# Performance work log

Measured on AMD Instinct MI355X. Metric: run time of the kernel, lower is better.

## Reference

```python
import jax, jax.numpy as jnp
import numpy as np

DIM = 1024
KV_DIM = 1024
WINDOW_SIZE = 64  # band half-width = 32, band width W = 65
B, S = 2, 2048


def setup_inputs() -> dict:
    key = jax.random.key(0)
    ks = jax.random.split(key, 12)
    w_scale = 1.0 / np.sqrt(DIM)
    return {
        "x": jax.random.normal(ks[0], (B, S, DIM), dtype=jnp.float32),
        # neural_memory: Linear(dim, kv) -> ReLU -> Linear(kv, dim); weights stored [in, out]
        "nm_w1": jax.random.normal(ks[1], (DIM, KV_DIM), dtype=jnp.float32) * w_scale,
        "nm_b1": jnp.zeros((KV_DIM,), dtype=jnp.float32),
        "nm_w2": jax.random.normal(ks[2], (KV_DIM, DIM), dtype=jnp.float32) * w_scale,
        "nm_b2": jnp.zeros((DIM,), dtype=jnp.float32),
        # SlidingWindowAttention projections (dim -> dim)
        "q_w": jax.random.normal(ks[3], (DIM, DIM), dtype=jnp.float32) * w_scale,
        "q_b": jnp.zeros((DIM,), dtype=jnp.float32),
        "k_w": jax.random.normal(ks[4], (DIM, DIM), dtype=jnp.float32) * w_scale,
        "k_b": jnp.zeros((DIM,), dtype=jnp.float32),
        "v_w": jax.random.normal(ks[5], (DIM, DIM), dtype=jnp.float32) * w_scale,
        "v_b": jnp.zeros((DIM,), dtype=jnp.float32),
    }


def _sliding_window_attention(m, q_w, q_b, k_w, k_b, v_w, v_b, window_size):
    # m: [B, S, D]. Per position i, attend to [i - w//2, i + w//2] inclusive.
    Bsz, Seq, D = m.shape
    q = m @ q_w + q_b
    k = m @ k_w + k_b
    v = m @ v_w + v_b
    half = window_size // 2
    offsets = jnp.arange(-half, half + 1)                # [W]
    idx = jnp.arange(Seq)[:, None] + offsets[None, :]    # [S, W]
    valid = (idx >= 0) & (idx < Seq)                     # [S, W]
    idx_c = jnp.clip(idx, 0, Seq - 1)
    k_band = k[:, idx_c]                                 # [B, S, W, D]
    v_band = v[:, idx_c]                                 # [B, S, W, D]
    scale = 1.0 / jnp.sqrt(jnp.float32(D))
    scores = jnp.einsum("bsd,bswd->bsw", q, k_band) * scale
    scores = jnp.where(valid[None, :, :], scores, -jnp.inf)
    weights = jax.nn.softmax(scores, axis=-1)            # [B, S, W]
    return jnp.einsum("bsw,bswd->bsd", weights, v_band)


def reference(x, nm_w1, nm_b1, nm_w2, nm_b2, q_w, q_b, k_w, k_b, v_w, v_b):
    # Faithful output path of LongTermMemory.forward: the key/value-proj MSE
    # surprise update mutates key_proj weights in-place (no_grad) but does NOT
    # affect the returned tensor o, which is swa(neural_memory(x)).
    h = jax.nn.relu(x @ nm_w1 + nm_b1)
    m = h @ nm_w2 + nm_b2                                # neural_memory(x): [B, S, D]
    return _sliding_window_attention(m, q_w, q_b, k_w, k_b, v_w, v_b, WINDOW_SIZE)
```

## Files before the change

kernel.cpp:

```cpp
#include <hip/hip_runtime.h>
#include <cstdint>

#define DIMN 1024
#define SEQ  2048
#define BATCH 2
#define MTOT (BATCH*SEQ)
#define NELEM_ACT (MTOT*DIMN)
#define NELEM_W   (DIMN*DIMN)

typedef __attribute__((ext_vector_type(8))) short   s16x8;
typedef __attribute__((ext_vector_type(4))) float   f32x4v;

__device__ __forceinline__ float b2f(unsigned short u) {
  union { unsigned int i; float f; } x; x.i = ((unsigned int)u) << 16; return x.f;
}
__device__ __forceinline__ unsigned short f2b(float f) {
  unsigned int x = __float_as_uint(f);
  return (unsigned short)((x + 0x7fffu + ((x >> 16) & 1u)) >> 16);
}

__device__ __forceinline__ void gload16(const void* g, void* l) {
  __builtin_amdgcn_global_load_lds((const __attribute__((address_space(1))) void*)g,
                                   (__attribute__((address_space(3))) void*)l,
                                   16, 0, 0);
}

__global__ __launch_bounds__(256) void cvt_kernel(
    const float* __restrict__ in, unsigned short* __restrict__ out, int n) {
  int i = (blockIdx.x * 256 + threadIdx.x) * 8;
  if (i >= n) return;
  float4 v0 = *(const float4*)(in + i);
  float4 v1 = *(const float4*)(in + i + 4);
  ushort4 a, b;
  a.x = f2b(v0.x); a.y = f2b(v0.y); a.z = f2b(v0.z); a.w = f2b(v0.w);
  b.x = f2b(v1.x); b.y = f2b(v1.y); b.z = f2b(v1.z); b.w = f2b(v1.w);
  *(ushort4*)(out + i) = a;
  *(ushort4*)(out + i + 4) = b;
}

__global__ __launch_bounds__(256) void transpose5_kernel(
    const float* __restrict__ w1, const float* __restrict__ w2,
    const float* __restrict__ qw, const float* __restrict__ kw,
    const float* __restrict__ vw,
    unsigned short* __restrict__ w1t, unsigned short* __restrict__ w2t,
    unsigned short* __restrict__ wqkvt) {
  __shared__ float t[32][33];
  int z = blockIdx.z;
  const float* in = (z == 0) ? w1 : (z == 1) ? w2 : (z == 2) ? qw : (z == 3) ? kw : vw;
  unsigned short* dst = (z == 0) ? w1t : (z == 1) ? w2t : wqkvt + (size_t)(z - 2) * NELEM_W;

  int tx = threadIdx.x & 31, ty = threadIdx.x >> 5;
  int r0 = blockIdx.y * 32, c0 = blockIdx.x * 32;
  #pragma unroll
  for (int i = 0; i < 32; i += 8)
    t[ty + i][tx] = in[(size_t)(r0 + ty + i) * DIMN + c0 + tx];
  __syncthreads();
  #pragma unroll
  for (int i = 0; i < 32; i += 8)
    dst[(size_t)(c0 + ty + i) * DIMN + r0 + tx] = f2b(t[tx][ty + i]);
}

template<int EPI>
__global__ __launch_bounds__(256) void gemm_kernel(
    const unsigned short* __restrict__ A, const unsigned short* __restrict__ Bt,
    const float* __restrict__ bias0, const float* __restrict__ bias1,
    const float* __restrict__ bias2,
    unsigned short* __restrict__ O, int Ndim, int Kdim) {
  __shared__ unsigned short lds[16 * 512];

  const int tid  = threadIdx.x;
  const int lane = tid & 63;
  const int wave = tid >> 6;
  const int wm = wave >> 1;
  const int wn = wave & 1;
  const int frow = lane & 15;
  const int krow = lane >> 4;
  const int bm0 = blockIdx.y * 128;
  const int bn0 = blockIdx.x * 128;

  f32x4v acc[4][4] = {};

  for (int k0 = 0; k0 < Kdim; k0 += 32) {
    for (int i = wave; i < 16; i += 4) {
      const unsigned short* src = (i < 8) ? A : Bt;
      int row = (i < 8) ? (bm0 + i * 16 + frow) : (bn0 + (i - 8) * 16 + frow);
      gload16(src + (size_t)row * Kdim + k0 + krow * 8, lds + i * 512);
    }
    __syncthreads();

    const short* sl = (const short*)lds;
    s16x8 a[4], b[4];
    #pragma unroll
    for (int m = 0; m < 4; ++m)
      a[m] = *(const s16x8*)(sl + (wm * 4 + m) * 512 + lane * 8);
    #pragma unroll
    for (int n = 0; n < 4; ++n)
      b[n] = *(const s16x8*)(sl + (8 + wn * 4 + n) * 512 + lane * 8);

    #pragma unroll
    for (int m = 0; m < 4; ++m)
      #pragma unroll
      for (int n = 0; n < 4; ++n)
        acc[m][n] = __builtin_amdgcn_mfma_f32_16x16x32_bf16(a[m], b[n], acc[m][n], 0, 0, 0);
    __syncthreads();
  }

  #pragma unroll
  for (int n = 0; n < 4; ++n) {
    int col = bn0 + wn * 64 + n * 16 + frow;
    float bv;
    if (EPI == 2) {
      int sel = col >> 10;
      const float* bp = (sel == 0) ? bias0 : (sel == 1) ? bias1 : bias2;
      bv = bp[col & (DIMN - 1)];
    } else {
      bv = bias0[col];
    }
    #pragma unroll
    for (int m = 0; m < 4; ++m) {
      int rbase = bm0 + wm * 64 + m * 16 + krow * 4;
      #pragma unroll
      for (int r = 0; r < 4; ++r) {
        float v = acc[m][n][r] + bv;
        if (EPI == 0) v = fmaxf(v, 0.f);
        O[(size_t)(rbase + r) * Ndim + col] = f2b(v);
      }
    }
  }
}

__global__ __launch_bounds__(256) void attn_kernel(
    const unsigned short* __restrict__ qkv, float* __restrict__ out) {
  __shared__ float sc[72];
  __shared__ float wts[72];
  __shared__ float part[4][16][68];
  const float NEG_INF = -__builtin_huge_valf();
  const int ROWS = 3 * DIMN;

  int bs = blockIdx.x;
  int s = bs & (SEQ - 1);
  int tid = threadIdx.x, lane = tid & 63, wave = tid >> 6;

  float qr[16];
  {
    const unsigned short* qp = qkv + (size_t)bs * ROWS + lane * 16;
    s16x8 q0 = *(const s16x8*)qp;
    s16x8 q1 = *(const s16x8*)(qp + 8);
    #pragma unroll
    for (int i = 0; i < 8; ++i) {
      qr[i]     = b2f((unsigned short)q0[i]) * 0.03125f;
      qr[8 + i] = b2f((unsigned short)q1[i]) * 0.03125f;
    }
  }

  const unsigned short* kbase = qkv + (size_t)(bs - s) * ROWS + DIMN;
  for (int j = wave; j < 65; j += 4) {
    int pos = s - 32 + j;
    float dot;
    if (pos >= 0 && pos < SEQ) {
      const unsigned short* kp = kbase + (size_t)pos * ROWS + lane * 16;
      s16x8 k0 = *(const s16x8*)kp;
      s16x8 k1 = *(const s16x8*)(kp + 8);
      dot = 0.f;
      #pragma unroll
      for (int i = 0; i < 8; ++i)
        dot += qr[i] * b2f((unsigned short)k0[i]) + qr[8 + i] * b2f((unsigned short)k1[i]);
      #pragma unroll
      for (int off = 32; off > 0; off >>= 1) dot += __shfl_xor(dot, off);
    } else {
      dot = NEG_INF;
    }
    if (lane == 0) sc[j] = dot;
  }
  __syncthreads();

  if (wave == 0) {
    float v0 = sc[lane];
    float v1 = (lane == 0) ? sc[64] : NEG_INF;
    float mx = fmaxf(v0, v1);
    #pragma unroll
    for (int off = 32; off > 0; off >>= 1) mx = fmaxf(mx, __shfl_xor(mx, off));
    float p0 = __expf(v0 - mx);
    float p1 = (lane == 0) ? __expf(v1 - mx) : 0.f;
    float sm = p0 + p1;
    #pragma unroll
    for (int off = 32; off > 0; off >>= 1) sm += __shfl_xor(sm, off);
    float inv = 1.f / sm;
    wts[lane] = p0 * inv;
    if (lane == 0) wts[64] = p1 * inv;
  }
  __syncthreads();

  float acc[16];
  #pragma unroll
  for (int i = 0; i < 16; ++i) acc[i] = 0.f;
  const unsigned short* vbase = qkv + (size_t)(bs - s) * ROWS + 2 * DIMN;
  for (int j = wave; j < 65; j += 4) {
    int pos = s - 32 + j;
    if (pos < 0 || pos >= SEQ) continue;
    float w = wts[j];
    const unsigned short* vp = vbase + (size_t)pos * ROWS + lane * 16;
    s16x8 v0 = *(const s16x8*)vp;
    s16x8 v1 = *(const s16x8*)(vp + 8);
    #pragma unroll
    for (int i = 0; i < 8; ++i) {
      acc[i]     += w * b2f((unsigned short)v0[i]);
      acc[8 + i] += w * b2f((unsigned short)v1[i]);
    }
  }
  #pragma unroll
  for (int i = 0; i < 16; ++i) part[wave][i][lane] = acc[i];
  __syncthreads();

  int d0 = tid * 4;
  int lsrc = d0 >> 4;
  int ibase = d0 & 15;
  float r0 = 0.f, r1 = 0.f, r2 = 0.f, r3 = 0.f;
  #pragma unroll
  for (int w = 0; w < 4; ++w) {
    r0 += part[w][ibase + 0][lsrc];
    r1 += part[w][ibase + 1][lsrc];
    r2 += part[w][ibase + 2][lsrc];
    r3 += part[w][ibase + 3][lsrc];
  }
  float4 r; r.x = r0; r.y = r1; r.z = r2; r.w = r3;
  *(float4*)(out + (size_t)bs * DIMN + d0) = r;
}

extern "C" void kernel_launch(void* const* d_in, const int* in_sizes, int n_in,
                              void* d_out, int out_size, void* d_ws, size_t ws_size,
                              hipStream_t stream) {
  const float* x  = (const float*)d_in[0];
  const float* w1 = (const float*)d_in[1];
  const float* b1 = (const float*)d_in[2];
  const float* w2 = (const float*)d_in[3];
  const float* b2 = (const float*)d_in[4];
  const float* qw = (const float*)d_in[5];
  const float* qb = (const float*)d_in[6];
  const float* kw = (const float*)d_in[7];
  const float* kb = (const float*)d_in[8];
  const float* vw = (const float*)d_in[9];
  const float* vb = (const float*)d_in[10];
  float* out = (float*)d_out;

  char* ws = (char*)d_ws;
  const size_t MB = 1024 * 1024;
  unsigned short* x_bf  = (unsigned short*)(ws);
  unsigned short* h_bf  = (unsigned short*)(ws + 8 * MB);
  unsigned short* qkv   = (unsigned short*)(ws);
  unsigned short* m_bf  = (unsigned short*)(ws + 24 * MB);
  unsigned short* w1t   = (unsigned short*)(ws + 32 * MB);
  unsigned short* w2t   = (unsigned short*)(ws + 34 * MB);
  unsigned short* wqkvt = (unsigned short*)(ws + 36 * MB);

  cvt_kernel<<<NELEM_ACT / (256 * 8), 256, 0, stream>>>(x, x_bf, NELEM_ACT);
  transpose5_kernel<<<dim3(32, 32, 5), 256, 0, stream>>>(w1, w2, qw, kw, vw,
                                                         w1t, w2t, wqkvt);

  dim3 g1(DIMN / 128, MTOT / 128);
  gemm_kernel<0><<<g1, 256, 0, stream>>>(x_bf, w1t, b1, nullptr, nullptr,
                                         h_bf, DIMN, DIMN);
  gemm_kernel<1><<<g1, 256, 0, stream>>>(h_bf, w2t, b2, nullptr, nullptr,
                                         m_bf, DIMN, DIMN);
  dim3 g2(3 * DIMN / 128, MTOT / 128);
  gemm_kernel<2><<<g2, 256, 0, stream>>>(m_bf, wqkvt, qb, kb, vb,
                                         qkv, 3 * DIMN, DIMN);

  attn_kernel<<<MTOT, 256, 0, stream>>>(qkv, out);
}
```

Baseline: 272.4 us.

## Rewrite sliding-window attention with MFMA blocks and retile GEMMs with K=64 steps

Replaces the per-token scalar attention kernel with a block kernel that handles 32 queries per workgroup. It computes the banded QK scores and the PV products with bf16 MFMA over a 96-key window, and the QKV GEMM epilogue writes V transposed so it can serve as the MFMA B operand. The GEMM kernel is templated on tile shape, uses a 64-deep K step per barrier pair, and the first two GEMMs move to 64x128 tiles for more workgroups. The band scheme computes about 50% redundant scores and quantizes the probabilities to bf16, and the transposed V stores are strided.

Result: faster. 242.1 us (-11.2%).

```diff
diff --git a/kernel.cpp b/kernel.cpp
--- a/kernel.cpp
+++ b/kernel.cpp
@@ -60,13 +60,15 @@
     dst[(size_t)(c0 + ty + i) * DIMN + r0 + tx] = f2b(t[tx][ty + i]);
 }
 
-template<int EPI>
+template<int MF, int NF, int EPI>
 __global__ __launch_bounds__(256) void gemm_kernel(
     const unsigned short* __restrict__ A, const unsigned short* __restrict__ Bt,
     const float* __restrict__ bias0, const float* __restrict__ bias1,
     const float* __restrict__ bias2,
-    unsigned short* __restrict__ O, int Ndim, int Kdim) {
-  __shared__ unsigned short lds[16 * 512];
+    unsigned short* __restrict__ O, unsigned short* __restrict__ O2,
+    int Ndim, int Kdim) {
+  constexpr int TB = (MF + NF) * 4;
+  __shared__ unsigned short lds[TB * 512];
 
   const int tid  = threadIdx.x;
   const int lane = tid & 63;
@@ -75,39 +77,50 @@
   const int wn = wave & 1;
   const int frow = lane & 15;
   const int krow = lane >> 4;
-  const int bm0 = blockIdx.y * 128;
-  const int bn0 = blockIdx.x * 128;
-
-  f32x4v acc[4][4] = {};
-
-  for (int k0 = 0; k0 < Kdim; k0 += 32) {
-    for (int i = wave; i < 16; i += 4) {
-      const unsigned short* src = (i < 8) ? A : Bt;
-      int row = (i < 8) ? (bm0 + i * 16 + frow) : (bn0 + (i - 8) * 16 + frow);
-      gload16(src + (size_t)row * Kdim + k0 + krow * 8, lds + i * 512);
+  const int bm0 = blockIdx.y * (MF * 32);
+  const int bn0 = blockIdx.x * (NF * 32);
+
+  f32x4v acc[MF][NF] = {};
+
+  for (int k0 = 0; k0 < Kdim; k0 += 64) {
+    #pragma unroll
+    for (int t = 0; t < TB / 4; ++t) {
+      int i = wave + t * 4;
+      const unsigned short* src;
+      if (i < MF * 4) {
+        int mf = i >> 1, ds = i & 1;
+        src = A + (size_t)(bm0 + mf * 16 + frow) * Kdim + k0 + ds * 32 + krow * 8;
+      } else {
+        int j = i - MF * 4;
+        int nf = j >> 1, ds = j & 1;
+        src = Bt + (size_t)(bn0 + nf * 16 + frow) * Kdim + k0 + ds * 32 + krow * 8;
+      }
+      gload16(src, lds + i * 512);
     }
     __syncthreads();
 
     const short* sl = (const short*)lds;
-    s16x8 a[4], b[4];
-    #pragma unroll
-    for (int m = 0; m < 4; ++m)
-      a[m] = *(const s16x8*)(sl + (wm * 4 + m) * 512 + lane * 8);
-    #pragma unroll
-    for (int n = 0; n < 4; ++n)
-      b[n] = *(const s16x8*)(sl + (8 + wn * 4 + n) * 512 + lane * 8);
-
-    #pragma unroll
-    for (int m = 0; m < 4; ++m)
-      #pragma unroll
-      for (int n = 0; n < 4; ++n)
-        acc[m][n] = __builtin_amdgcn_mfma_f32_16x16x32_bf16(a[m], b[n], acc[m][n], 0, 0, 0);
-    __syncthreads();
-  }
-
-  #pragma unroll
-  for (int n = 0; n < 4; ++n) {
-    int col = bn0 + wn * 64 + n * 16 + frow;
+    #pragma unroll
+    for (int ds = 0; ds < 2; ++ds) {
+      s16x8 a[MF], b[NF];
+      #pragma unroll
+      for (int m = 0; m < MF; ++m)
+        a[m] = *(const s16x8*)(sl + ((wm * MF + m) * 2 + ds) * 512 + lane * 8);
+      #pragma unroll
+      for (int n = 0; n < NF; ++n)
+        b[n] = *(const s16x8*)(sl + (MF * 4 + (wn * NF + n) * 2 + ds) * 512 + lane * 8);
+      #pragma unroll
+      for (int m = 0; m < MF; ++m)
+        #pragma unroll
+        for (int n = 0; n < NF; ++n)
+          acc[m][n] = __builtin_amdgcn_mfma_f32_16x16x32_bf16(a[m], b[n], acc[m][n], 0, 0, 0);
+    }
+    __syncthreads();
+  }
+
+  #pragma unroll
+  for (int n = 0; n < NF; ++n) {
+    int col = bn0 + wn * (NF * 16) + n * 16 + frow;
     float bv;
     if (EPI == 2) {
       int sel = col >> 10;
@@ -117,114 +130,173 @@
       bv = bias0[col];
     }
     #pragma unroll
-    for (int m = 0; m < 4; ++m) {
-      int rbase = bm0 + wm * 64 + m * 16 + krow * 4;
+    for (int m = 0; m < MF; ++m) {
+      int rbase = bm0 + wm * (MF * 16) + m * 16 + krow * 4;
+      if (EPI == 2 && col >= 2048) {
+        int d = col - 2048;
+        ushort4 pk;
+        pk.x = f2b(acc[m][n][0] + bv); pk.y = f2b(acc[m][n][1] + bv);
+        pk.z = f2b(acc[m][n][2] + bv); pk.w = f2b(acc[m][n][3] + bv);
+        *(ushort4*)(O2 + (size_t)d * MTOT + rbase) = pk;
+      } else {
+        #pragma unroll
+        for (int r = 0; r < 4; ++r) {
+          float v = acc[m][n][r] + bv;
+          if (EPI == 0) v = fmaxf(v, 0.f);
+          if (EPI == 2) O[(size_t)(rbase + r) * 2048 + col] = f2b(v);
+          else          O[(size_t)(rbase + r) * Ndim + col] = f2b(v);
+        }
+      }
+    }
+  }
+}
+
+#define QBLK 32
+#define NEGI (-1.0e30f)
+
+__global__ __launch_bounds__(256) void attn_mfma_kernel(
+    const unsigned short* __restrict__ qk,
+    const unsigned short* __restrict__ vt,
+    float* __restrict__ out) {
+  __shared__ unsigned short stage[24 * 512];
+  __shared__ unsigned short plds[QBLK][136];
+  __shared__ float pmax[2][QBLK];
+  __shared__ float psum[2][QBLK];
+
+  const int tid = threadIdx.x, lane = tid & 63, wave = tid >> 6;
+  const int frow = lane & 15, krow = lane >> 4;
+  const int tok0 = blockIdx.x * QBLK;
+  const int s0 = tok0 & (SEQ - 1);
+  const int bbase = tok0 - s0;
+  const int qf = wave & 1;
+  const int kh = wave >> 1;
+
+  f32x4v sacc[3] = {};
+  for (int d0 = 0; d0 < DIMN; d0 += 64) {
+    #pragma unroll
+    for (int t = 0; t < 4; ++t) {
+      int i = wave + t * 4;
+      const unsigned short* src;
+      if (i < 4) {
+        int qfs = i >> 1, ds = i & 1;
+        src = qk + (size_t)(tok0 + qfs * 16 + frow) * 2048 + d0 + ds * 32 + krow * 8;
+      } else {
+        int j = i - 4;
+        int kf = j >> 1, ds = j & 1;
+        int kpos = s0 - 32 + kf * 16 + frow;
+        kpos = min(max(kpos, 0), SEQ - 1);
+        src = qk + (size_t)(bbase + kpos) * 2048 + 1024 + d0 + ds * 32 + krow * 8;
+      }
+      gload16(src, stage + i * 512);
+    }
+    __syncthreads();
+    const short* sl = (const short*)stage;
+    #pragma unroll
+    for (int ds = 0; ds < 2; ++ds) {
+      s16x8 bq = *(const s16x8*)(sl + (qf * 2 + ds) * 512 + lane * 8);
+      #pragma unroll
+      for (int f = 0; f < 3; ++f) {
+        int kf = kh * 3 + f;
+        s16x8 ak = *(const s16x8*)(sl + (4 + kf * 2 + ds) * 512 + lane * 8);
+        sacc[f] = __builtin_amdgcn_mfma_f32_16x16x32_bf16(ak, bq, sacc[f], 0, 0, 0);
+      }
+    }
+    __syncthreads();
+  }
+
+  const int qloc = qf * 16 + frow;
+  const int qpos = s0 + qloc;
+  float sv[3][4];
+  float mx = NEGI;
+  #pragma unroll
+  for (int f = 0; f < 3; ++f) {
+    #pragma unroll
+    for (int r = 0; r < 4; ++r) {
+      int kloc = (kh * 3 + f) * 16 + krow * 4 + r;
+      int kpos = s0 - 32 + kloc;
+      int dd = kpos - qpos;
+      bool valid = (dd >= -32) && (dd <= 32) && (kpos >= 0) && (kpos < SEQ);
+      float v = valid ? sacc[f][r] * 0.03125f : NEGI;
+      sv[f][r] = v;
+      mx = fmaxf(mx, v);
+    }
+  }
+  mx = fmaxf(mx, __shfl_xor(mx, 16));
+  mx = fmaxf(mx, __shfl_xor(mx, 32));
+  if (lane < 16) pmax[kh][qf * 16 + lane] = mx;
+  __syncthreads();
+  float M = fmaxf(pmax[0][qloc], pmax[1][qloc]);
+  float sum = 0.f;
+  unsigned int pw[3][2];
+  #pragma unroll
+  for (int f = 0; f < 3; ++f) {
+    #pragma unroll
+    for (int pr = 0; pr < 2; ++pr) {
+      float p0 = __expf(sv[f][2 * pr]     - M);
+      float p1 = __expf(sv[f][2 * pr + 1] - M);
+      sum += p0 + p1;
+      pw[f][pr] = (unsigned int)f2b(p0) | ((unsigned int)f2b(p1) << 16);
+    }
+  }
+  sum += __shfl_xor(sum, 16);
+  sum += __shfl_xor(sum, 32);
+  if (lane < 16) psum[kh][qf * 16 + lane] = sum;
+  {
+    unsigned int* pl = (unsigned int*)&plds[0][0];
+    int base = qloc * 68 + (kh * 3) * 8 + krow * 2;
+    #pragma unroll
+    for (int f = 0; f < 3; ++f) {
+      pl[base + f * 8 + 0] = pw[f][0];
+      pl[base + f * 8 + 1] = pw[f][1];
+    }
+  }
+  __syncthreads();
+
+  s16x8 pa[3];
+  #pragma unroll
+  for (int kf = 0; kf < 3; ++kf)
+    pa[kf] = *(const s16x8*)((const short*)&plds[0][0] +
+                             (qf * 16 + frow) * 136 + kf * 32 + krow * 8);
+  float rden[4];
+  #pragma unroll
+  for (int r = 0; r < 4; ++r) {
+    int q = qf * 16 + krow * 4 + r;
+    rden[r] = 1.f / (psum[0][q] + psum[1][q]);
+  }
+
+  for (int c = 0; c < 8; ++c) {
+    #pragma unroll
+    for (int t = 0; t < 6; ++t) {
+      int i = wave + t * 4;
+      int kf = i >> 3, nf = i & 7;
+      int d = c * 128 + nf * 16 + frow;
+      int tt = s0 - 32 + kf * 32 + krow * 8;
+      tt = min(max(tt, 0), SEQ - 8);
+      gload16(vt + (size_t)d * MTOT + bbase + tt, stage + i * 512);
+    }
+    __syncthreads();
+    const short* sl = (const short*)stage;
+    f32x4v oacc[4] = {};
+    #pragma unroll
+    for (int kf = 0; kf < 3; ++kf) {
+      #pragma unroll
+      for (int n = 0; n < 4; ++n) {
+        int nf = kh * 4 + n;
+        s16x8 bv = *(const s16x8*)(sl + (kf * 8 + nf) * 512 + lane * 8);
+        oacc[n] = __builtin_amdgcn_mfma_f32_16x16x32_bf16(pa[kf], bv, oacc[n], 0, 0, 0);
+      }
+    }
+    #pragma unroll
+    for (int n = 0; n < 4; ++n) {
+      int d = c * 128 + (kh * 4 + n) * 16 + frow;
       #pragma unroll
       for (int r = 0; r < 4; ++r) {
-        float v = acc[m][n][r] + bv;
-        if (EPI == 0) v = fmaxf(v, 0.f);
-        O[(size_t)(rbase + r) * Ndim + col] = f2b(v);
-      }
-    }
-  }
-}
-
-__global__ __launch_bounds__(256) void attn_kernel(
-    const unsigned short* __restrict__ qkv, float* __restrict__ out) {
-  __shared__ float sc[72];
-  __shared__ float wts[72];
-  __shared__ float part[4][16][68];
-  const float NEG_INF = -__builtin_huge_valf();
-  const int ROWS = 3 * DIMN;
-
-  int bs = blockIdx.x;
-  int s = bs & (SEQ - 1);
-  int tid = threadIdx.x, lane = tid & 63, wave = tid >> 6;
-
-  float qr[16];
-  {
-    const unsigned short* qp = qkv + (size_t)bs * ROWS + lane * 16;
-    s16x8 q0 = *(const s16x8*)qp;
-    s16x8 q1 = *(const s16x8*)(qp + 8);
-    #pragma unroll
-    for (int i = 0; i < 8; ++i) {
-      qr[i]     = b2f((unsigned short)q0[i]) * 0.03125f;
-      qr[8 + i] = b2f((unsigned short)q1[i]) * 0.03125f;
-    }
-  }
-
-  const unsigned short* kbase = qkv + (size_t)(bs - s) * ROWS + DIMN;
-  for (int j = wave; j < 65; j += 4) {
-    int pos = s - 32 + j;
-    float dot;
-    if (pos >= 0 && pos < SEQ) {
-      const unsigned short* kp = kbase + (size_t)pos * ROWS + lane * 16;
-      s16x8 k0 = *(const s16x8*)kp;
-      s16x8 k1 = *(const s16x8*)(kp + 8);
-      dot = 0.f;
-      #pragma unroll
-      for (int i = 0; i < 8; ++i)
-        dot += qr[i] * b2f((unsigned short)k0[i]) + qr[8 + i] * b2f((unsigned short)k1[i]);
-      #pragma unroll
-      for (int off = 32; off > 0; off >>= 1) dot += __shfl_xor(dot, off);
-    } else {
-      dot = NEG_INF;
-    }
-    if (lane == 0) sc[j] = dot;
-  }
-  __syncthreads();
-
-  if (wave == 0) {
-    float v0 = sc[lane];
-    float v1 = (lane == 0) ? sc[64] : NEG_INF;
-    float mx = fmaxf(v0, v1);
-    #pragma unroll
-    for (int off = 32; off > 0; off >>= 1) mx = fmaxf(mx, __shfl_xor(mx, off));
-    float p0 = __expf(v0 - mx);
-    float p1 = (lane == 0) ? __expf(v1 - mx) : 0.f;
-    float sm = p0 + p1;
-    #pragma unroll
-    for (int off = 32; off > 0; off >>= 1) sm += __shfl_xor(sm, off);
-    float inv = 1.f / sm;
-    wts[lane] = p0 * inv;
-    if (lane == 0) wts[64] = p1 * inv;
-  }
-  __syncthreads();
-
-  float acc[16];
-  #pragma unroll
-  for (int i = 0; i < 16; ++i) acc[i] = 0.f;
-  const unsigned short* vbase = qkv + (size_t)(bs - s) * ROWS + 2 * DIMN;
-  for (int j = wave; j < 65; j += 4) {
-    int pos = s - 32 + j;
-    if (pos < 0 || pos >= SEQ) continue;
-    float w = wts[j];
-    const unsigned short* vp = vbase + (size_t)pos * ROWS + lane * 16;
-    s16x8 v0 = *(const s16x8*)vp;
-    s16x8 v1 = *(const s16x8*)(vp + 8);
-    #pragma unroll
-    for (int i = 0; i < 8; ++i) {
-      acc[i]     += w * b2f((unsigned short)v0[i]);
-      acc[8 + i] += w * b2f((unsigned short)v1[i]);
-    }
-  }
-  #pragma unroll
-  for (int i = 0; i < 16; ++i) part[wave][i][lane] = acc[i];
-  __syncthreads();
-
-  int d0 = tid * 4;
-  int lsrc = d0 >> 4;
-  int ibase = d0 & 15;
-  float r0 = 0.f, r1 = 0.f, r2 = 0.f, r3 = 0.f;
-  #pragma unroll
-  for (int w = 0; w < 4; ++w) {
-    r0 += part[w][ibase + 0][lsrc];
-    r1 += part[w][ibase + 1][lsrc];
-    r2 += part[w][ibase + 2][lsrc];
-    r3 += part[w][ibase + 3][lsrc];
-  }
-  float4 r; r.x = r0; r.y = r1; r.z = r2; r.w = r3;
-  *(float4*)(out + (size_t)bs * DIMN + d0) = r;
+        int q = qf * 16 + krow * 4 + r;
+        out[(size_t)(tok0 + q) * DIMN + d] = oacc[n][r] * rden[r];
+      }
+    }
+    __syncthreads();
+  }
 }
 
 extern "C" void kernel_launch(void* const* d_in, const int* in_sizes, int n_in,
@@ -246,25 +318,26 @@
   char* ws = (char*)d_ws;
   const size_t MB = 1024 * 1024;
   unsigned short* x_bf  = (unsigned short*)(ws);
-  unsigned short* h_bf  = (unsigned short*)(ws + 8 * MB);
-  unsigned short* qkv   = (unsigned short*)(ws);
-  unsigned short* m_bf  = (unsigned short*)(ws + 24 * MB);
-  unsigned short* w1t   = (unsigned short*)(ws + 32 * MB);
-  unsigned short* w2t   = (unsigned short*)(ws + 34 * MB);
-  unsigned short* wqkvt = (unsigned short*)(ws + 36 * MB);
+  unsigned short* h_bf  = (unsigned short*)(ws + 8  * MB);
+  unsigned short* m_bf  = (unsigned short*)(ws + 16 * MB);
+  unsigned short* qkbuf = (unsigned short*)(ws + 24 * MB);
+  unsigned short* vtbuf = (unsigned short*)(ws + 40 * MB);
+  unsigned short* w1t   = (unsigned short*)(ws + 48 * MB);
+  unsigned short* w2t   = (unsigned short*)(ws + 50 * MB);
+  unsigned short* wqkvt = (unsigned short*)(ws + 52 * MB);
 
   cvt_kernel<<<NELEM_ACT / (256 * 8), 256, 0, stream>>>(x, x_bf, NELEM_ACT);
   transpose5_kernel<<<dim3(32, 32, 5), 256, 0, stream>>>(w1, w2, qw, kw, vw,
                                                          w1t, w2t, wqkvt);
 
-  dim3 g1(DIMN / 128, MTOT / 128);
-  gemm_kernel<0><<<g1, 256, 0, stream>>>(x_bf, w1t, b1, nullptr, nullptr,
-                                         h_bf, DIMN, DIMN);
-  gemm_kernel<1><<<g1, 256, 0, stream>>>(h_bf, w2t, b2, nullptr, nullptr,
-                                         m_bf, DIMN, DIMN);
+  dim3 g1(DIMN / 128, MTOT / 64);
+  gemm_kernel<2, 4, 0><<<g1, 256, 0, stream>>>(x_bf, w1t, b1, nullptr, nullptr,
+                                               h_bf, nullptr, DIMN, DIMN);
+  gemm_kernel<2, 4, 1><<<g1, 256, 0, stream>>>(h_bf, w2t, b2, nullptr, nullptr,
+                                               m_bf, nullptr, DIMN, DIMN);
   dim3 g2(3 * DIMN / 128, MTOT / 128);
-  gemm_kernel<2><<<g2, 256, 0, stream>>>(m_bf, wqkvt, qb, kb, vb,
-                                         qkv, 3 * DIMN, DIMN);
-
-  attn_kernel<<<MTOT, 256, 0, stream>>>(qkv, out);
-}
+  gemm_kernel<4, 4, 2><<<g2, 256, 0, stream>>>(m_bf, wqkvt, qb, kb, vb,
+                                               qkbuf, vtbuf, 3 * DIMN, DIMN);
+
+  attn_mfma_kernel<<<MTOT / QBLK, 256, 0, stream>>>(qkbuf, vtbuf, out);
+}
```
